# Kernel optimization log

Hardware: AMD Instinct MI355X
Metric: run time of the kernel (lower is better)

The kernel has to match this reference:

```python
import jax, jax.numpy as jnp
import numpy as np
from jax import lax

D = 256      # d_model
NH = 4       # nhead == len(multi_size)
DH = D // NH # per-head dim = 64
B, H, W = 8, 32, 32
EPS_LN = 1e-5
EPS_ATT = 1e-6


def conv2d(x, w, pad):
    # x: [B,C,H,W], w: [O,I,k,k], SAME padding via pad=k//2
    return lax.conv_general_dilated(
        x, w, window_strides=(1, 1), padding=[(pad, pad), (pad, pad)],
        dimension_numbers=("NCHW", "OIHW", "NCHW"))


def layer_norm(x, g, b):
    m = jnp.mean(x, axis=-1, keepdims=True)
    v = jnp.mean((x - m) ** 2, axis=-1, keepdims=True)
    return (x - m) * lax.rsqrt(v + EPS_LN) * g + b


def setup_inputs() -> dict:
    key = jax.random.key(0)
    ks = jax.random.split(key, 20)
    s = 0.02
    inp = {
        "x": jax.random.normal(ks[0], (B, D, H, W), jnp.float32),
        "source": jax.random.normal(ks[1], (B, D, H, W), jnp.float32),
        # q projection: conv3x3 d_model -> d_model (bias-free)
        "Wq": jax.random.normal(ks[2], (D, D, 3, 3), jnp.float32) * s,
        # MultiConv k projection: kernels 1,3,5,7, each d_model -> dim
        "Wk1": jax.random.normal(ks[3], (DH, D, 1, 1), jnp.float32) * s,
        "Wk3": jax.random.normal(ks[4], (DH, D, 3, 3), jnp.float32) * s,
        "Wk5": jax.random.normal(ks[5], (DH, D, 5, 5), jnp.float32) * s,
        "Wk7": jax.random.normal(ks[6], (DH, D, 7, 7), jnp.float32) * s,
        # MultiConv v projection
        "Wv1": jax.random.normal(ks[7], (DH, D, 1, 1), jnp.float32) * s,
        "Wv3": jax.random.normal(ks[8], (DH, D, 3, 3), jnp.float32) * s,
        "Wv5": jax.random.normal(ks[9], (DH, D, 5, 5), jnp.float32) * s,
        "Wv7": jax.random.normal(ks[10], (DH, D, 7, 7), jnp.float32) * s,
        # merge linear (bias=False), stored [in,out]
        "Wm": jax.random.normal(ks[11], (D, D), jnp.float32) * s,
        "ln1_g": jnp.ones((D,), jnp.float32),
        "ln1_b": jnp.zeros((D,), jnp.float32),
        "ln2_g": jnp.ones((D,), jnp.float32),
        "ln2_b": jnp.zeros((D,), jnp.float32),
        # FF mlp: Linear(2D->2D, no bias), ReLU, Linear(2D->D, no bias); [in,out]
        "W1": jax.random.normal(ks[12], (2 * D, 2 * D), jnp.float32) * s,
        "W2": jax.random.normal(ks[13], (2 * D, D), jnp.float32) * s,
    }
    return inp


def _forward(x, source, Wq, Wk1, Wk3, Wk5, Wk7, Wv1, Wv3, Wv5, Wv7,
             Wm, ln1_g, ln1_b, ln2_g, ln2_b, W1, W2):
    b, c, h, w = x.shape
    h1, w1 = source.shape[2], source.shape[3]
    L = h * w
    S = h1 * w1

    # projections (multi-scale convs -> heads along channel)
    q = conv2d(x, Wq, 1)                                        # [b,D,h,w]
    k = jnp.concatenate([conv2d(source, Wk1, 0), conv2d(source, Wk3, 1),
                         conv2d(source, Wk5, 2), conv2d(source, Wk7, 3)], axis=1)
    v = jnp.concatenate([conv2d(source, Wv1, 0), conv2d(source, Wv3, 1),
                         conv2d(source, Wv5, 2), conv2d(source, Wv7, 3)], axis=1)

    # b c h w -> b (h w) (nhead dim) -> b L nhead dim
    q = q.transpose(0, 2, 3, 1).reshape(b, L, NH, DH)
    k = k.transpose(0, 2, 3, 1).reshape(b, S, NH, DH)
    v = v.transpose(0, 2, 3, 1).reshape(b, S, NH, DH)

    # FullAttention_vis: softmax attention map [b, L, S, nhead]
    temp = DH ** -0.5
    qk = jnp.einsum("blhd,bshd->blsh", q, k)
    attn_vis = jax.nn.softmax(qk * temp, axis=2)

    # LinearAttention (elu+1 kernel feature map)
    Qf = jax.nn.elu(q) + 1.0
    Kf = jax.nn.elu(k) + 1.0
    v_len = jnp.float32(S)
    vals = v / v_len
    KV = jnp.einsum("bshd,bshv->bhdv", Kf, vals)                # [b,NH,DH,DH]
    Z = 1.0 / (jnp.einsum("blhd,bhd->blh", Qf, Kf.sum(axis=1)) + EPS_ATT)
    msg = jnp.einsum("blhd,bhdv,blh->blhv", Qf, KV, Z) * v_len  # [b,L,NH,DH]

    # merge + norm1
    msg = layer_norm(msg.reshape(b, L, D) @ Wm, ln1_g, ln1_b)

    # FF (mlp): cat -> Linear -> ReLU -> Linear -> norm2
    xf = x.transpose(0, 2, 3, 1).reshape(b, L, c)
    ff = jax.nn.relu(jnp.concatenate([xf, msg], axis=2) @ W1) @ W2
    msg = layer_norm(ff, ln2_g, ln2_b)                          # [b,L,D]
    msg = msg.reshape(b, h, w, c).transpose(0, 3, 1, 2)         # b c h w

    out = x + msg
    # b (h0 w0) (h1 w1) c -> b c h0 w0 h1 w1
    vis = attn_vis.reshape(b, h, w, h1, w1, NH).transpose(0, 5, 1, 2, 3, 4)
    return out, vis


def reference(x, source, Wq, Wk1, Wk3, Wk5, Wk7, Wv1, Wv3, Wv5, Wv7,
              Wm, ln1_g, ln1_b, ln2_g, ln2_b, W1, W2):
    return _forward(x, source, Wq, Wk1, Wk3, Wk5, Wk7, Wv1, Wv3, Wv5, Wv7,
                    Wm, ln1_g, ln1_b, ln2_g, ln2_b, W1, W2)
```

## Files before the change

### kernel.cpp

```cpp
#include <hip/hip_runtime.h>

#define DEV __device__ __forceinline__

typedef unsigned short u16;
typedef unsigned int u32;
typedef __bf16 bf16x8 __attribute__((ext_vector_type(8)));
typedef float f32x4 __attribute__((ext_vector_type(4)));

DEV float elu1(float x) { return x > 0.f ? x + 1.f : __expf(x); }

DEV u16 f2bf(float f) {
    union { float f; unsigned u; } v; v.f = f;
    unsigned r = v.u + 0x7fffu + ((v.u >> 16) & 1u);
    return (u16)(r >> 16);
}

__global__ __launch_bounds__(256) void repack_kernel(
    const float* __restrict__ Wq,
    const float* __restrict__ Wk1, const float* __restrict__ Wk3,
    const float* __restrict__ Wk5, const float* __restrict__ Wk7,
    const float* __restrict__ Wv1, const float* __restrict__ Wv3,
    const float* __restrict__ Wv5, const float* __restrict__ Wv7,
    u16* __restrict__ wpack)
{
    int gid = blockIdx.x * 256 + threadIdx.x;
    int frag = gid >> 6, l = gid & 63;
    const float* W; int K, ocbase = 0, rel;
    if (frag < 1152) {
        W = Wq; K = 3; int slot = frag / 288; rel = frag % 288; ocbase = slot * 64;
    } else {
        int f = frag - 1152; int side = f / 2688; f %= 2688;
        if (f < 32)        { W = side ? Wv1 : Wk1; K = 1; rel = f; }
        else if (f < 320)  { W = side ? Wv3 : Wk3; K = 3; rel = f - 32; }
        else if (f < 1120) { W = side ? Wv5 : Wk5; K = 5; rel = f - 320; }
        else               { W = side ? Wv7 : Wk7; K = 7; rel = f - 1120; }
    }
    int og = rel & 3, cc = (rel >> 2) & 7, tap = rel >> 5;
    int dy = tap / K, dx = tap % K;
    int oc = ocbase + og * 16 + (l & 15);
    int c0 = cc * 32 + (l >> 4) * 8;
    u16 pk[8];
#pragma unroll
    for (int j = 0; j < 8; ++j)
        pk[j] = f2bf(W[((size_t)(oc * 256 + c0 + j) * K + dy) * K + dx]);
    *(int4*)&wpack[(size_t)frag * 512 + l * 8] = *(const int4*)pk;
}

__global__ __launch_bounds__(256) void cast_src_kernel(
    const float* __restrict__ x, const float* __restrict__ src,
    u16* __restrict__ xbh, u16* __restrict__ sbh)
{
    __shared__ float lds[32 * 129];
    const int i = blockIdx.x, t = threadIdx.x;
    const int inp = i >> 9, rem = i & 511;
    const int b = rem >> 6, cc = (rem >> 3) & 7, pxb = rem & 7;
    const float* in = (inp ? src : x) + ((size_t)b * 256 + cc * 32) * 1024 + pxb * 128;
    u16* outp = (inp ? sbh : xbh) + (size_t)b * 262144 + (size_t)cc * 32768 + pxb * 128 * 32;
#pragma unroll
    for (int u = 0; u < 4; ++u) {
        int unit = t + u * 256;
        int r = unit >> 5, px4 = unit & 31;
        float4 v = *(const float4*)(in + (size_t)r * 1024 + px4 * 4);
        lds[r * 129 + px4 * 4 + 0] = v.x;
        lds[r * 129 + px4 * 4 + 1] = v.y;
        lds[r * 129 + px4 * 4 + 2] = v.z;
        lds[r * 129 + px4 * 4 + 3] = v.w;
    }
    __syncthreads();
#pragma unroll
    for (int u = 0; u < 2; ++u) {
        int unit = t + u * 256;
        int px = unit >> 2, cg = unit & 3;
        u16 pk[8];
#pragma unroll
        for (int j = 0; j < 8; ++j) pk[j] = f2bf(lds[(cg * 8 + j) * 129 + px]);
        *(int4*)&outp[px * 32 + cg * 8] = *(const int4*)pk;
    }
}

__global__ __launch_bounds__(256) void cast_qk_kernel(
    const float* __restrict__ qb, const float* __restrict__ kb,
    u16* __restrict__ qbt, u16* __restrict__ kbt)
{
    __shared__ float lds[64 * 65];
    const int i = blockIdx.x, t = threadIdx.x;
    const int inp = i >> 9, rem = i & 511;
    const int b = rem >> 6, h = (rem >> 4) & 3, pxb = rem & 15;
    const float* in = (inp ? kb : qb) + ((size_t)b * 256 + h * 64) * 1024 + pxb * 64;
    u16* outp = (inp ? kbt : qbt) + (((size_t)(b * 4 + h)) * 1024 + pxb * 64) * 64;
#pragma unroll
    for (int u = 0; u < 4; ++u) {
        int unit = t + u * 256;
        int r = unit >> 4, px4 = unit & 15;
        float4 v = *(const float4*)(in + (size_t)r * 1024 + px4 * 4);
        lds[r * 65 + px4 * 4 + 0] = v.x;
        lds[r * 65 + px4 * 4 + 1] = v.y;
        lds[r * 65 + px4 * 4 + 2] = v.z;
        lds[r * 65 + px4 * 4 + 3] = v.w;
    }
    __syncthreads();
#pragma unroll
    for (int u = 0; u < 2; ++u) {
        int unit = t + u * 256;
        int px = unit >> 3, cg = unit & 7;
        u16 pk[8];
#pragma unroll
        for (int j = 0; j < 8; ++j) pk[j] = f2bf(lds[(cg * 8 + j) * 65 + px]);
        *(int4*)&outp[px * 64 + cg * 8] = *(const int4*)pk;
    }
}

__global__ __launch_bounds__(256) void repack_ff_kernel(
    const float* __restrict__ W1, const float* __restrict__ W2,
    const float* __restrict__ Wm,
    u16* __restrict__ w1p, u16* __restrict__ w2p, u16* __restrict__ wmp)
{
    int gid = blockIdx.x * 256 + threadIdx.x;
    int f = gid >> 6, l = gid & 63;
    if (f >= 896) return;
    u16 pk[8];
    if (f < 512) {
        int ks = f >> 5, nf = f & 31;
#pragma unroll
        for (int j = 0; j < 8; ++j)
            pk[j] = f2bf(W1[(size_t)(ks * 32 + (l >> 4) * 8 + j) * 512 + nf * 16 + (l & 15)]);
        *(int4*)&w1p[(size_t)f * 512 + l * 8] = *(const int4*)pk;
    } else if (f < 768) {
        int f2 = f - 512;
        int ks = f2 >> 4, nf = f2 & 15;
#pragma unroll
        for (int j = 0; j < 8; ++j)
            pk[j] = f2bf(W2[(size_t)(ks * 32 + (l >> 4) * 8 + j) * 256 + nf * 16 + (l & 15)]);
        *(int4*)&w2p[(size_t)f2 * 512 + l * 8] = *(const int4*)pk;
    } else {
        int f3 = f - 768;
        int ks = f3 >> 4, nf = f3 & 15;
#pragma unroll
        for (int j = 0; j < 8; ++j)
            pk[j] = f2bf(Wm[(size_t)(ks * 32 + (l >> 4) * 8 + j) * 256 + nf * 16 + (l & 15)]);
        *(int4*)&wmp[(size_t)f3 * 512 + l * 8] = *(const int4*)pk;
    }
}

template<int K>
DEV void conv_mfma_body(const u16* __restrict__ srcb,
                        const u16* __restrict__ wsec,
                        float* __restrict__ dst,
                        u16* Bt, int y0, int cch0, int ncc, int t)
{
    constexpr int P = K / 2;
    const int w = t >> 6, l = t & 63;
    const int chi = l >> 4, ln = l & 15;
    const int rowbase = chi * 22 + w * 2 + 3 - P;
    const int colbase = ln + 3 - P;
    f32x4 acc[4][4];
#pragma unroll
    for (int m = 0; m < 4; ++m)
#pragma unroll
        for (int n = 0; n < 4; ++n) acc[m][n] = (f32x4){0.f, 0.f, 0.f, 0.f};

    for (int cc = 0; cc < ncc; ++cc) {
        const int ccg = cch0 + cc;
        __syncthreads();
#pragma unroll
        for (int u = 0; u < 7; ++u) {
            int unit = t + (u << 9);
            if (unit < 2816) {
                int xv = unit & 31, r = unit >> 5;
                int yy = r % 22, ch = r / 22;
                int ygl = y0 - 3 + yy;
                int4 pk;
                if ((unsigned)ygl < 32u)
                    pk = *(const int4*)&srcb[(size_t)ccg * 32768 + (ygl * 32 + xv) * 32 + ch * 8];
// ... 59 lines not shown
    const int bx = blockIdx.x, t = threadIdx.x;
    const int g = bx & 31, b = (bx >> 5) & 7, m = bx >> 8;
    if (g < 4) {
        conv_mfma_body<3>(xbh + (size_t)b * 262144,
                          wpack + (size_t)(g * 288) * 512,
                          qb + ((size_t)b * 256 + g * 64) * 1024,
                          Bt, m * 16, 0, 8, t);
        return;
    }
    const int gs = g - 4;
    const int side = gs / 14, gg = gs % 14;
    const u16* sp = sbh + (size_t)b * 262144;
    float* fin = side ? vb : kb;
    const size_t wkb = 1152 + (size_t)side * 2688;
    if (gg == 0) {
        conv_mfma_body<1>(sp, wpack + (wkb + 0) * 512,
                          fin + ((size_t)b * 256) * 1024, Bt, m * 16, 0, 8, t);
    } else if (gg == 1) {
        conv_mfma_body<3>(sp, wpack + (wkb + 32) * 512,
                          fin + ((size_t)b * 256 + 64) * 1024, Bt, m * 16, 0, 8, t);
    } else if (gg < 6) {
        int cpart = gg - 2;
        conv_mfma_body<5>(sp, wpack + (wkb + 320) * 512,
                          p5 + (((size_t)side * 4 + cpart) * 8 + b) * 65536,
                          Bt, m * 16, cpart * 2, 2, t);
    } else {
        int cpart = gg - 6;
        conv_mfma_body<7>(sp, wpack + (wkb + 1120) * 512,
                          p7 + (((size_t)side * 8 + cpart) * 8 + b) * 65536,
                          Bt, m * 16, cpart, 1, t);
    }
}

__global__ __launch_bounds__(256) void reduce_kernel(
    const float* __restrict__ p5, const float* __restrict__ p7,
    float* __restrict__ kb, float* __restrict__ vb)
{
    int gid = blockIdx.x * 256 + threadIdx.x;
    int px4 = gid & 255;
    int rr = gid >> 8;
    int oc = rr & 63, b = (rr >> 6) & 7, head = (rr >> 9) & 1, side = rr >> 10;
    float* outb = side ? vb : kb;
    float4 s = make_float4(0.f, 0.f, 0.f, 0.f);
    if (head == 0) {
#pragma unroll
        for (int p = 0; p < 4; ++p) {
            float4 u = *((const float4*)(p5 + (((size_t)side * 4 + p) * 8 + b) * 65536 + (size_t)oc * 1024) + px4);
            s.x += u.x; s.y += u.y; s.z += u.z; s.w += u.w;
        }
        *((float4*)(outb + ((size_t)b * 256 + 128 + oc) * 1024) + px4) = s;
    } else {
#pragma unroll
        for (int p = 0; p < 8; ++p) {
            float4 u = *((const float4*)(p7 + (((size_t)side * 8 + p) * 8 + b) * 65536 + (size_t)oc * 1024) + px4);
            s.x += u.x; s.y += u.y; s.z += u.z; s.w += u.w;
        }
        *((float4*)(outb + ((size_t)b * 256 + 192 + oc) * 1024) + px4) = s;
    }
}

__global__ __launch_bounds__(512) void qk_sm_kernel(const u16* __restrict__ qbt,
                                                    const u16* __restrict__ kbt,
                                                    float* __restrict__ vis)
{
    __shared__ u16 shbuf[36 * 512];
    __shared__ float redM[32 * 8];
    __shared__ float redS[32 * 8];
    u16* kf = shbuf;
    u16* qf = shbuf + 32 * 512;
    const int t = threadIdx.x;
    const int bx = blockIdx.x;
    const int b = bx >> 7, h = (bx >> 5) & 3, l0 = (bx & 31) * 32;
    const u16* qtp = qbt + ((size_t)(b * 4 + h)) * 1024 * 64;
    const u16* ktp = kbt + ((size_t)(b * 4 + h)) * 1024 * 64;

    if (t < 256) {
        int r = t & 31, dblk = t >> 5;
        int4 pk = *(const int4*)&qtp[(size_t)(l0 + r) * 64 + dblk * 8];
        *(int4*)&qf[(((r >> 4) * 2 + (dblk >> 2)) * 64 + (dblk & 3) * 16 + (r & 15)) * 8] = pk;
    }
    __syncthreads();

    const int w = t >> 6, l = t & 63, ln = l & 15, lg = l >> 4;
    bf16x8 a[2][2];
#pragma unroll
    for (int fr = 0; fr < 2; ++fr)
#pragma unroll
        for (int ks = 0; ks < 2; ++ks)
            a[fr][ks] = *(const bf16x8*)&qf[((fr * 2 + ks) * 64 + l) * 8];

    f32x4 acc[2][4][2];
#pragma unroll
    for (int fr = 0; fr < 2; ++fr)
#pragma unroll
        for (int cc = 0; cc < 4; ++cc)
#pragma unroll
            for (int f = 0; f < 2; ++f) acc[fr][cc][f] = (f32x4){0.f, 0.f, 0.f, 0.f};

#pragma unroll
    for (int cc = 0; cc < 4; ++cc) {
        __syncthreads();
#pragma unroll
        for (int it = 0; it < 4; ++it) {
            int unit = it * 512 + t;
            int sl = unit & 255, dblk = unit >> 8;
            int4 pk = *(const int4*)&ktp[(size_t)(cc * 256 + sl) * 64 + dblk * 8];
            *(int4*)&kf[(((sl >> 4) * 2 + (dblk >> 2)) * 64 + (dblk & 3) * 16 + (sl & 15)) * 8] = pk;
        }
        __syncthreads();
#pragma unroll
        for (int f = 0; f < 2; ++f) {
            int fg = (w * 2 + f) * 2;
            bf16x8 b0 = *(const bf16x8*)&kf[((fg + 0) * 64 + l) * 8];
            bf16x8 b1 = *(const bf16x8*)&kf[((fg + 1) * 64 + l) * 8];
#pragma unroll
            for (int fr = 0; fr < 2; ++fr) {
                acc[fr][cc][f] = __builtin_amdgcn_mfma_f32_16x16x32_bf16(a[fr][0], b0, acc[fr][cc][f], 0, 0, 0);
                acc[fr][cc][f] = __builtin_amdgcn_mfma_f32_16x16x32_bf16(a[fr][1], b1, acc[fr][cc][f], 0, 0, 0);
            }
        }
    }

#pragma unroll
    for (int fr = 0; fr < 2; ++fr)
#pragma unroll
        for (int cc = 0; cc < 4; ++cc)
#pragma unroll
            for (int f = 0; f < 2; ++f)
#pragma unroll
                for (int e = 0; e < 4; ++e) acc[fr][cc][f][e] *= 0.125f;

    float rmax[2][4];
#pragma unroll
    for (int fr = 0; fr < 2; ++fr)
#pragma unroll
        for (int reg = 0; reg < 4; ++reg) {
            float m = -1e30f;
#pragma unroll
            for (int cc = 0; cc < 4; ++cc)
#pragma unroll
                for (int f = 0; f < 2; ++f) m = fmaxf(m, acc[fr][cc][f][reg]);
#pragma unroll
            for (int off = 1; off < 16; off <<= 1) m = fmaxf(m, __shfl_xor(m, off));
            if (ln == 0) redM[(fr * 16 + lg * 4 + reg) * 8 + w] = m;
            rmax[fr][reg] = m;
        }
    __syncthreads();
#pragma unroll
    for (int fr = 0; fr < 2; ++fr)
#pragma unroll
        for (int reg = 0; reg < 4; ++reg) {
            int r = fr * 16 + lg * 4 + reg;
            float m = redM[r * 8];
#pragma unroll
            for (int ww = 1; ww < 8; ++ww) m = fmaxf(m, redM[r * 8 + ww]);
            rmax[fr][reg] = m;
        }
#pragma unroll
    for (int fr = 0; fr < 2; ++fr)
#pragma unroll
        for (int reg = 0; reg < 4; ++reg) {
            float s = 0.f;
            float m = rmax[fr][reg];
#pragma unroll
            for (int cc = 0; cc < 4; ++cc)
#pragma unroll
                for (int f = 0; f < 2; ++f) {
                    float e = __expf(acc[fr][cc][f][reg] - m);
                    acc[fr][cc][f][reg] = e;
                    s += e;
                }
#pragma unroll
            for (int off = 1; off < 16; off <<= 1) s += __shfl_xor(s, off);
            if (ln == 0) redS[(fr * 16 + lg * 4 + reg) * 8 + w] = s;
        }
    __syncthreads();
    float invv[2][4];
#pragma unroll
    for (int fr = 0; fr < 2; ++fr)
#pragma unroll
        for (int reg = 0; reg < 4; ++reg) {
            int r = fr * 16 + lg * 4 + reg;
            float s = redS[r * 8] + redS[r * 8 + 1] + redS[r * 8 + 2] + redS[r * 8 + 3]
                    + redS[r * 8 + 4] + redS[r * 8 + 5] + redS[r * 8 + 6] + redS[r * 8 + 7];
            invv[fr][reg] = 1.f / s;
        }
    float* outT = (float*)shbuf;
    float* visp = vis + (((size_t)(b * 4 + h)) << 20);
#pragma unroll
    for (int cc = 0; cc < 4; ++cc) {
        __syncthreads();
#pragma unroll
        for (int fr = 0; fr < 2; ++fr)
#pragma unroll
            for (int reg = 0; reg < 4; ++reg) {
                int r = fr * 16 + lg * 4 + reg;
#pragma unroll
                for (int f = 0; f < 2; ++f)
                    outT[r * 260 + w * 32 + f * 16 + ln] = acc[fr][cc][f][reg] * invv[fr][reg];
            }
        __syncthreads();
#pragma unroll
        for (int u = 0; u < 4; ++u) {
            int unit = u * 512 + t;
            int r = unit >> 6, c4 = unit & 63;
            float4 v = *(const float4*)&outT[r * 260 + c4 * 4];
            *(float4*)&visp[(size_t)(l0 + r) * 1024 + cc * 256 + c4 * 4] = v;
        }
    }
}

__global__ __launch_bounds__(256) void kv_kernel(const float* __restrict__ k,
                                                 const float* __restrict__ v,
                                                 float* __restrict__ KVp,
                                                 float* __restrict__ Ksump)
{
    __shared__ float4 Kt4[64*17];
    __shared__ float4 Vt4[64*16];
    float* Kt = (float*)Kt4;
    float* Vt = (float*)Vt4;
    const int t = threadIdx.x;
    const int bx = blockIdx.x;
    const int b = bx >> 4, h = (bx >> 2) & 3, ch = bx & 3;
    const float* kb = k + ((size_t)b*256 + h*64)*1024 + ch*256;
    const float* vb = v + ((size_t)b*256 + h*64)*1024 + ch*256;
    const int d = t >> 2, v0 = (t & 3) * 16;
    float4 acc[4];
#pragma unroll
    for (int j = 0; j < 4; ++j) acc[j] = make_float4(0.f, 0.f, 0.f, 0.f);
    float ks = 0.f;
    for (int st = 0; st < 4; ++st) {
        __syncthreads();
        {
            int dd = t >> 2, r0 = (t & 3) * 16;
#pragma unroll
            for (int mm = 0; mm < 4; ++mm) {
                float4 kv = *(const float4*)(kb + dd*1024 + st*64 + r0 + mm*4);
                Kt[(r0+mm*4+0)*68 + dd] = elu1(kv.x);
                Kt[(r0+mm*4+1)*68 + dd] = elu1(kv.y);
                Kt[(r0+mm*4+2)*68 + dd] = elu1(kv.z);
                Kt[(r0+mm*4+3)*68 + dd] = elu1(kv.w);
                float4 vv = *(const float4*)(vb + dd*1024 + st*64 + r0 + mm*4);
                Vt[(r0+mm*4+0)*64 + dd] = vv.x;
                Vt[(r0+mm*4+1)*64 + dd] = vv.y;
                Vt[(r0+mm*4+2)*64 + dd] = vv.z;
                Vt[(r0+mm*4+3)*64 + dd] = vv.w;
            }
        }
        __syncthreads();
#pragma unroll 8
        for (int s = 0; s < 64; ++s) {
            float kf = Kt[s*68 + d];
            const float4* vp = (const float4*)(Vt + s*64 + v0);
#pragma unroll
            for (int j = 0; j < 4; ++j) {
                float4 vv = vp[j];
                acc[j].x += kf*vv.x; acc[j].y += kf*vv.y;
                acc[j].z += kf*vv.z; acc[j].w += kf*vv.w;
            }
        }
        if (t < 64) {
#pragma unroll 8
            for (int s = 0; s < 64; ++s) ks += Kt[s*68 + t];
        }
    }
    float* op = KVp + ((size_t)((ch*32 + b*4 + h)*64 + d))*64 + v0;
#pragma unroll
    for (int j = 0; j < 4; ++j) ((float4*)op)[j] = acc[j];
    if (t < 64) Ksump[(size_t)(ch*32 + b*4 + h)*64 + t] = ks;
}

__global__ __launch_bounds__(256) void msg_kernel(const float* __restrict__ q,
                                                  const float* __restrict__ KVp,
                                                  const float* __restrict__ Ksump,
                                                  float* __restrict__ msg)
{
    __shared__ float4 kvl4[4*1028];
    __shared__ float ksl[4*65];
    float* kvl = (float*)kvl4;
    const int t = threadIdx.x;
    const int bx = blockIdx.x;
    const int b = bx >> 4;
    const int l0 = (bx & 15) * 64;
    for (int m = 0; m < 64; ++m) {
        int idx = t + 256*m;
        int hh = idx >> 12, dd = (idx >> 6) & 63, vv = idx & 63;
        float s = 0.f;
#pragma unroll
        for (int ch = 0; ch < 4; ++ch)
            s += KVp[(size_t)((ch*32 + b*4))*4096 + idx];
        kvl[hh*4112 + dd*64 + vv] = s;
    }
    {
        float s = 0.f;
#pragma unroll
        for (int ch = 0; ch < 4; ++ch)
            s += Ksump[(size_t)(ch*32 + b*4)*64 + t];
        ksl[(t >> 6)*65 + (t & 63)] = s;
    }
    __syncthreads();
    const int h = t & 3, l = l0 + (t >> 2);
    const float* qb = q + ((size_t)b*256 + h*64)*1024 + l;
    float qf[64];
#pragma unroll
    for (int dd = 0; dd < 64; ++dd) qf[dd] = elu1(qb[dd*1024]);
    float zd = 1e-6f;
#pragma unroll
    for (int dd = 0; dd < 64; ++dd) zd += qf[dd] * ksl[h*65 + dd];
    const float Z = 1.f / zd;
    float* op = msg + ((size_t)(b*1024 + l))*256 + h*64;
    for (int c0 = 0; c0 < 64; c0 += 16) {
        float4 a[4];
#pragma unroll
        for (int j = 0; j < 4; ++j) a[j] = make_float4(0.f, 0.f, 0.f, 0.f);
#pragma unroll
        for (int dd = 0; dd < 64; ++dd) {
            float qv = qf[dd];
            const float4* kp = (const float4*)(kvl + h*4112 + dd*64 + c0);
#pragma unroll
            for (int j = 0; j < 4; ++j) {
                float4 kk = kp[j];
                a[j].x += qv*kk.x; a[j].y += qv*kk.y;
                a[j].z += qv*kk.z; a[j].w += qv*kk.w;
            }
        }
#pragma unroll
        for (int j = 0; j < 4; ++j) {
            a[j].x *= Z; a[j].y *= Z; a[j].z *= Z; a[j].w *= Z;
            ((float4*)(op + c0))[j] = a[j];
        }
    }
}

__global__ __launch_bounds__(256) void ff_fused_kernel(
    const float* __restrict__ x, const float* __restrict__ msg,
    const u16* __restrict__ wmp,
    const u16* __restrict__ w1p, const u16* __restrict__ w2p,
    const float* __restrict__ g1, const float* __restrict__ b1,
    const float* __restrict__ g2, const float* __restrict__ b2,
    float* __restrict__ out)
{
    __shared__ u16 tile[16 * 520];
    __shared__ u16 mtile[16 * 264];
    __shared__ float redS[16 * 4];
    __shared__ float redQ[16 * 4];
    float* tf = (float*)tile;
    const int t = threadIdx.x;
    const int base = blockIdx.x * 16;
    const int b = base >> 10, l0 = base & 1023;
    const int w = t >> 6, l = t & 63, ln = l & 15, lg = l >> 4;

    {
        int rr = t & 15, cg = t >> 4;
        for (int cci = 0; cci < 16; ++cci) {
            int c = cci * 16 + cg;
            tile[rr * 520 + c] = f2bf(x[((size_t)b * 256 + c) * 1024 + l0 + rr]);
// ... 159 lines not shown
    const float* Wk3  = (const float*)d_in[4];
    const float* Wk5  = (const float*)d_in[5];
    const float* Wk7  = (const float*)d_in[6];
    const float* Wv1  = (const float*)d_in[7];
    const float* Wv3  = (const float*)d_in[8];
    const float* Wv5  = (const float*)d_in[9];
    const float* Wv7  = (const float*)d_in[10];
    const float* Wm   = (const float*)d_in[11];
    const float* g1   = (const float*)d_in[12];
    const float* b1   = (const float*)d_in[13];
    const float* g2   = (const float*)d_in[14];
    const float* b2   = (const float*)d_in[15];
    const float* W1   = (const float*)d_in[16];
    const float* W2   = (const float*)d_in[17];

    float* out = (float*)d_out;
    float* vis = out + 2097152;

    float* p5 = vis;
    float* p7 = vis + 4194304;

    float* ws    = (float*)d_ws;
    float* qb    = ws;
    float* kb    = ws + 2097152;
    float* vb    = ws + 4194304;
    u16*   wpack = (u16*)(ws + 6291456);
    u16*   w1p   = (u16*)(ws + 6291456);
    u16*   w2p   = (u16*)(ws + 6422528);
    u16*   wmp   = (u16*)(ws + 6488064);
    u16*   qbt   = (u16*)(ws + 6520832);
    u16*   kbt   = (u16*)(ws + 7569408);
    u16*   xbh   = (u16*)(ws + 7962624);
    u16*   sbh   = (u16*)(ws + 9011200);
    float* msg   = ws + 7962624;
    float* KVp   = ws + 12156928;
    float* Ksump = ws + 12681216;

    repack_kernel   <<<1632, 256, 0, stream>>>(Wq, Wk1, Wk3, Wk5, Wk7,
                                               Wv1, Wv3, Wv5, Wv7, wpack);
    cast_src_kernel <<<1024, 256, 0, stream>>>(x, src, xbh, sbh);
    conv_mfma_kernel<<<512,  512, 0, stream>>>(xbh, sbh, wpack, qb, kb, vb, p5, p7);
    reduce_kernel   <<<2048, 256, 0, stream>>>(p5, p7, kb, vb);
    repack_ff_kernel<<<224,  256, 0, stream>>>(W1, W2, Wm, w1p, w2p, wmp);
    cast_qk_kernel  <<<1024, 256, 0, stream>>>(qb, kb, qbt, kbt);
    qk_sm_kernel    <<<1024, 512, 0, stream>>>(qbt, kbt, vis);
    kv_kernel       <<<128,  256, 0, stream>>>(kb, vb, KVp, Ksump);
    msg_kernel      <<<128,  256, 0, stream>>>(qb, KVp, Ksump, msg);
    ff_fused_kernel <<<512,  256, 0, stream>>>(x, msg, wmp, w1p, w2p,
                                               g1, b1, g2, b2, out);
}
```

Before: 274.1 us.

## Merge independent small kernels into fused launches via block-index dispatch

Independent kernels are combined into single launches that branch on blockIdx: weight repack with input cast, partial-sum reduce with FF weight repack, q/k cast with the KV reduction, and QK softmax with the message computation. This cuts the launch count from ten to six and lets unrelated work run concurrently on the GPU. The message path now reads bf16-transposed q instead of fp32 q, which lowers precision slightly and changes the memory access pattern. The msg buffer is moved so it no longer overlaps xbh and sbh.

New measurement: 269.1 us. Within noise of the previous version (-1.8%).

```diff
diff --git a/kernel.cpp b/kernel.cpp
--- a/kernel.cpp
+++ b/kernel.cpp
@@ -15,43 +15,47 @@
     return (u16)(r >> 16);
 }
 
-__global__ __launch_bounds__(256) void repack_kernel(
+DEV float bf2f(u16 h) {
+    union { u32 u; float f; } v; v.u = ((u32)h) << 16; return v.f;
+}
+
+__global__ __launch_bounds__(256) void prep1_kernel(
     const float* __restrict__ Wq,
     const float* __restrict__ Wk1, const float* __restrict__ Wk3,
     const float* __restrict__ Wk5, const float* __restrict__ Wk7,
     const float* __restrict__ Wv1, const float* __restrict__ Wv3,
     const float* __restrict__ Wv5, const float* __restrict__ Wv7,
-    u16* __restrict__ wpack)
-{
-    int gid = blockIdx.x * 256 + threadIdx.x;
-    int frag = gid >> 6, l = gid & 63;
-    const float* W; int K, ocbase = 0, rel;
-    if (frag < 1152) {
-        W = Wq; K = 3; int slot = frag / 288; rel = frag % 288; ocbase = slot * 64;
-    } else {
-        int f = frag - 1152; int side = f / 2688; f %= 2688;
-        if (f < 32)        { W = side ? Wv1 : Wk1; K = 1; rel = f; }
-        else if (f < 320)  { W = side ? Wv3 : Wk3; K = 3; rel = f - 32; }
-        else if (f < 1120) { W = side ? Wv5 : Wk5; K = 5; rel = f - 320; }
-        else               { W = side ? Wv7 : Wk7; K = 7; rel = f - 1120; }
-    }
-    int og = rel & 3, cc = (rel >> 2) & 7, tap = rel >> 5;
-    int dy = tap / K, dx = tap % K;
-    int oc = ocbase + og * 16 + (l & 15);
-    int c0 = cc * 32 + (l >> 4) * 8;
-    u16 pk[8];
-#pragma unroll
-    for (int j = 0; j < 8; ++j)
-        pk[j] = f2bf(W[((size_t)(oc * 256 + c0 + j) * K + dy) * K + dx]);
-    *(int4*)&wpack[(size_t)frag * 512 + l * 8] = *(const int4*)pk;
-}
-
-__global__ __launch_bounds__(256) void cast_src_kernel(
+    u16* __restrict__ wpack,
     const float* __restrict__ x, const float* __restrict__ src,
     u16* __restrict__ xbh, u16* __restrict__ sbh)
 {
     __shared__ float lds[32 * 129];
-    const int i = blockIdx.x, t = threadIdx.x;
+    const int t = threadIdx.x;
+    if (blockIdx.x < 1632) {
+        int gid = blockIdx.x * 256 + t;
+        int frag = gid >> 6, l = gid & 63;
+        const float* W; int K, ocbase = 0, rel;
+        if (frag < 1152) {
+            W = Wq; K = 3; int slot = frag / 288; rel = frag % 288; ocbase = slot * 64;
+        } else {
+            int f = frag - 1152; int side = f / 2688; f %= 2688;
+            if (f < 32)        { W = side ? Wv1 : Wk1; K = 1; rel = f; }
+            else if (f < 320)  { W = side ? Wv3 : Wk3; K = 3; rel = f - 32; }
+            else if (f < 1120) { W = side ? Wv5 : Wk5; K = 5; rel = f - 320; }
+            else               { W = side ? Wv7 : Wk7; K = 7; rel = f - 1120; }
+        }
+        int og = rel & 3, cc = (rel >> 2) & 7, tap = rel >> 5;
+        int dy = tap / K, dx = tap % K;
+        int oc = ocbase + og * 16 + (l & 15);
+        int c0 = cc * 32 + (l >> 4) * 8;
+        u16 pk[8];
+#pragma unroll
+        for (int j = 0; j < 8; ++j)
+            pk[j] = f2bf(W[((size_t)(oc * 256 + c0 + j) * K + dy) * K + dx]);
+        *(int4*)&wpack[(size_t)frag * 512 + l * 8] = *(const int4*)pk;
+        return;
+    }
+    const int i = blockIdx.x - 1632;
     const int inp = i >> 9, rem = i & 511;
     const int b = rem >> 6, cc = (rem >> 3) & 7, pxb = rem & 7;
     const float* in = (inp ? src : x) + ((size_t)b * 256 + cc * 32) * 1024 + pxb * 128;
@@ -75,70 +79,6 @@
 #pragma unroll
         for (int j = 0; j < 8; ++j) pk[j] = f2bf(lds[(cg * 8 + j) * 129 + px]);
         *(int4*)&outp[px * 32 + cg * 8] = *(const int4*)pk;
-    }
-}
-
-__global__ __launch_bounds__(256) void cast_qk_kernel(
-    const float* __restrict__ qb, const float* __restrict__ kb,
-    u16* __restrict__ qbt, u16* __restrict__ kbt)
-{
-    __shared__ float lds[64 * 65];
-    const int i = blockIdx.x, t = threadIdx.x;
-    const int inp = i >> 9, rem = i & 511;
-    const int b = rem >> 6, h = (rem >> 4) & 3, pxb = rem & 15;
-    const float* in = (inp ? kb : qb) + ((size_t)b * 256 + h * 64) * 1024 + pxb * 64;
-    u16* outp = (inp ? kbt : qbt) + (((size_t)(b * 4 + h)) * 1024 + pxb * 64) * 64;
-#pragma unroll
-    for (int u = 0; u < 4; ++u) {
-        int unit = t + u * 256;
-        int r = unit >> 4, px4 = unit & 15;
-        float4 v = *(const float4*)(in + (size_t)r * 1024 + px4 * 4);
-        lds[r * 65 + px4 * 4 + 0] = v.x;
-        lds[r * 65 + px4 * 4 + 1] = v.y;
-        lds[r * 65 + px4 * 4 + 2] = v.z;
-        lds[r * 65 + px4 * 4 + 3] = v.w;
-    }
-    __syncthreads();
-#pragma unroll
-    for (int u = 0; u < 2; ++u) {
-        int unit = t + u * 256;
-        int px = unit >> 3, cg = unit & 7;
-        u16 pk[8];
-#pragma unroll
-        for (int j = 0; j < 8; ++j) pk[j] = f2bf(lds[(cg * 8 + j) * 65 + px]);
-        *(int4*)&outp[px * 64 + cg * 8] = *(const int4*)pk;
-    }
-}
-
-__global__ __launch_bounds__(256) void repack_ff_kernel(
-    const float* __restrict__ W1, const float* __restrict__ W2,
-    const float* __restrict__ Wm,
-    u16* __restrict__ w1p, u16* __restrict__ w2p, u16* __restrict__ wmp)
-{
-    int gid = blockIdx.x * 256 + threadIdx.x;
-    int f = gid >> 6, l = gid & 63;
-    if (f >= 896) return;
-    u16 pk[8];
-    if (f < 512) {
-        int ks = f >> 5, nf = f & 31;
-#pragma unroll
-        for (int j = 0; j < 8; ++j)
-            pk[j] = f2bf(W1[(size_t)(ks * 32 + (l >> 4) * 8 + j) * 512 + nf * 16 + (l & 15)]);
-        *(int4*)&w1p[(size_t)f * 512 + l * 8] = *(const int4*)pk;
-    } else if (f < 768) {
-        int f2 = f - 512;
-        int ks = f2 >> 4, nf = f2 & 15;
-#pragma unroll
-        for (int j = 0; j < 8; ++j)
-            pk[j] = f2bf(W2[(size_t)(ks * 32 + (l >> 4) * 8 + j) * 256 + nf * 16 + (l & 15)]);
-        *(int4*)&w2p[(size_t)f2 * 512 + l * 8] = *(const int4*)pk;
-    } else {
-        int f3 = f - 768;
-        int ks = f3 >> 4, nf = f3 & 15;
-#pragma unroll
-        for (int j = 0; j < 8; ++j)
-            pk[j] = f2bf(Wm[(size_t)(ks * 32 + (l >> 4) * 8 + j) * 256 + nf * 16 + (l & 15)]);
-        *(int4*)&wmp[(size_t)f3 * 512 + l * 8] = *(const int4*)pk;
     }
 }
 
@@ -264,198 +204,110 @@
     }
 }
 
-__global__ __launch_bounds__(256) void reduce_kernel(
+__global__ __launch_bounds__(256) void prep2_kernel(
     const float* __restrict__ p5, const float* __restrict__ p7,
-    float* __restrict__ kb, float* __restrict__ vb)
+    float* __restrict__ kb, float* __restrict__ vb,
+    const float* __restrict__ W1, const float* __restrict__ W2,
+    const float* __restrict__ Wm,
+    u16* __restrict__ w1p, u16* __restrict__ w2p, u16* __restrict__ wmp)
 {
-    int gid = blockIdx.x * 256 + threadIdx.x;
-    int px4 = gid & 255;
-    int rr = gid >> 8;
-    int oc = rr & 63, b = (rr >> 6) & 7, head = (rr >> 9) & 1, side = rr >> 10;
-    float* outb = side ? vb : kb;
-    float4 s = make_float4(0.f, 0.f, 0.f, 0.f);
-    if (head == 0) {
-#pragma unroll
-        for (int p = 0; p < 4; ++p) {
-            float4 u = *((const float4*)(p5 + (((size_t)side * 4 + p) * 8 + b) * 65536 + (size_t)oc * 1024) + px4);
-            s.x += u.x; s.y += u.y; s.z += u.z; s.w += u.w;
-        }
-        *((float4*)(outb + ((size_t)b * 256 + 128 + oc) * 1024) + px4) = s;
+    const int t = threadIdx.x;
+    if (blockIdx.x < 2048) {
+        int gid = blockIdx.x * 256 + t;
+        int px4 = gid & 255;
+        int rr = gid >> 8;
+        int oc = rr & 63, b = (rr >> 6) & 7, head = (rr >> 9) & 1, side = rr >> 10;
+        float* outb = side ? vb : kb;
+        float4 s = make_float4(0.f, 0.f, 0.f, 0.f);
+        if (head == 0) {
+#pragma unroll
+            for (int p = 0; p < 4; ++p) {
+                float4 u = *((const float4*)(p5 + (((size_t)side * 4 + p) * 8 + b) * 65536 + (size_t)oc * 1024) + px4);
+                s.x += u.x; s.y += u.y; s.z += u.z; s.w += u.w;
+            }
+            *((float4*)(outb + ((size_t)b * 256 + 128 + oc) * 1024) + px4) = s;
+        } else {
+#pragma unroll
+            for (int p = 0; p < 8; ++p) {
+                float4 u = *((const float4*)(p7 + (((size_t)side * 8 + p) * 8 + b) * 65536 + (size_t)oc * 1024) + px4);
+                s.x += u.x; s.y += u.y; s.z += u.z; s.w += u.w;
+            }
+            *((float4*)(outb + ((size_t)b * 256 + 192 + oc) * 1024) + px4) = s;
+        }
+        return;
+    }
+    int gid = (blockIdx.x - 2048) * 256 + t;
+    int f = gid >> 6, l = gid & 63;
+    if (f >= 896) return;
+    u16 pk[8];
+    if (f < 512) {
+        int ks = f >> 5, nf = f & 31;
+#pragma unroll
+        for (int j = 0; j < 8; ++j)
+            pk[j] = f2bf(W1[(size_t)(ks * 32 + (l >> 4) * 8 + j) * 512 + nf * 16 + (l & 15)]);
+        *(int4*)&w1p[(size_t)f * 512 + l * 8] = *(const int4*)pk;
+    } else if (f < 768) {
+        int f2 = f - 512;
+        int ks = f2 >> 4, nf = f2 & 15;
+#pragma unroll
+        for (int j = 0; j < 8; ++j)
+            pk[j] = f2bf(W2[(size_t)(ks * 32 + (l >> 4) * 8 + j) * 256 + nf * 16 + (l & 15)]);
+        *(int4*)&w2p[(size_t)f2 * 512 + l * 8] = *(const int4*)pk;
     } else {
-#pragma unroll
-        for (int p = 0; p < 8; ++p) {
-            float4 u = *((const float4*)(p7 + (((size_t)side * 8 + p) * 8 + b) * 65536 + (size_t)oc * 1024) + px4);
-            s.x += u.x; s.y += u.y; s.z += u.z; s.w += u.w;
-        }
-        *((float4*)(outb + ((size_t)b * 256 + 192 + oc) * 1024) + px4) = s;
-    }
-}
-
-__global__ __launch_bounds__(512) void qk_sm_kernel(const u16* __restrict__ qbt,
-                                                    const u16* __restrict__ kbt,
-                                                    float* __restrict__ vis)
+        int f3 = f - 768;
+        int ks = f3 >> 4, nf = f3 & 15;
+#pragma unroll
+        for (int j = 0; j < 8; ++j)
+            pk[j] = f2bf(Wm[(size_t)(ks * 32 + (l >> 4) * 8 + j) * 256 + nf * 16 + (l & 15)]);
+        *(int4*)&wmp[(size_t)f3 * 512 + l * 8] = *(const int4*)pk;
+    }
+}
+
+__global__ __launch_bounds__(256) void prep3_kernel(
+    const float* __restrict__ qb, const float* __restrict__ kb,
+    const float* __restrict__ vb,
+    u16* __restrict__ qbt, u16* __restrict__ kbt,
+    float* __restrict__ KVp, float* __restrict__ Ksump)
 {
-    __shared__ u16 shbuf[36 * 512];
-    __shared__ float redM[32 * 8];
-    __shared__ float redS[32 * 8];
-    u16* kf = shbuf;
-    u16* qf = shbuf + 32 * 512;
+    __shared__ float4 smem4[2112];
     const int t = threadIdx.x;
-    const int bx = blockIdx.x;
-    const int b = bx >> 7, h = (bx >> 5) & 3, l0 = (bx & 31) * 32;
-    const u16* qtp = qbt + ((size_t)(b * 4 + h)) * 1024 * 64;
-    const u16* ktp = kbt + ((size_t)(b * 4 + h)) * 1024 * 64;
-
-    if (t < 256) {
-        int r = t & 31, dblk = t >> 5;
-        int4 pk = *(const int4*)&qtp[(size_t)(l0 + r) * 64 + dblk * 8];
-        *(int4*)&qf[(((r >> 4) * 2 + (dblk >> 2)) * 64 + (dblk & 3) * 16 + (r & 15)) * 8] = pk;
-    }
-    __syncthreads();
-
-    const int w = t >> 6, l = t & 63, ln = l & 15, lg = l >> 4;
-    bf16x8 a[2][2];
-#pragma unroll
-    for (int fr = 0; fr < 2; ++fr)
-#pragma unroll
-        for (int ks = 0; ks < 2; ++ks)
-            a[fr][ks] = *(const bf16x8*)&qf[((fr * 2 + ks) * 64 + l) * 8];
-
-    f32x4 acc[2][4][2];
-#pragma unroll
-    for (int fr = 0; fr < 2; ++fr)
-#pragma unroll
-        for (int cc = 0; cc < 4; ++cc)
-#pragma unroll
-            for (int f = 0; f < 2; ++f) acc[fr][cc][f] = (f32x4){0.f, 0.f, 0.f, 0.f};
-
-#pragma unroll
-    for (int cc = 0; cc < 4; ++cc) {
+    if (blockIdx.x < 1024) {
+        float* lds = (float*)smem4;
+        const int i = blockIdx.x;
+        const int inp = i >> 9, rem = i & 511;
+        const int b = rem >> 6, h = (rem >> 4) & 3, pxb = rem & 15;
+        const float* in = (inp ? kb : qb) + ((size_t)b * 256 + h * 64) * 1024 + pxb * 64;
+        u16* outp = (inp ? kbt : qbt) + (((size_t)(b * 4 + h)) * 1024 + pxb * 64) * 64;
+#pragma unroll
+        for (int u = 0; u < 4; ++u) {
+            int unit = t + u * 256;
+            int r = unit >> 4, px4 = unit & 15;
+            float4 v = *(const float4*)(in + (size_t)r * 1024 + px4 * 4);
+            lds[r * 65 + px4 * 4 + 0] = v.x;
+            lds[r * 65 + px4 * 4 + 1] = v.y;
+            lds[r * 65 + px4 * 4 + 2] = v.z;
+            lds[r * 65 + px4 * 4 + 3] = v.w;
+        }
         __syncthreads();
 #pragma unroll
-        for (int it = 0; it < 4; ++it) {
-            int unit = it * 512 + t;
-            int sl = unit & 255, dblk = unit >> 8;
-            int4 pk = *(const int4*)&ktp[(size_t)(cc * 256 + sl) * 64 + dblk * 8];
-            *(int4*)&kf[(((sl >> 4) * 2 + (dblk >> 2)) * 64 + (dblk & 3) * 16 + (sl & 15)) * 8] = pk;
-        }
-        __syncthreads();
-#pragma unroll
-        for (int f = 0; f < 2; ++f) {
-            int fg = (w * 2 + f) * 2;
-            bf16x8 b0 = *(const bf16x8*)&kf[((fg + 0) * 64 + l) * 8];
-            bf16x8 b1 = *(const bf16x8*)&kf[((fg + 1) * 64 + l) * 8];
-#pragma unroll
-            for (int fr = 0; fr < 2; ++fr) {
-                acc[fr][cc][f] = __builtin_amdgcn_mfma_f32_16x16x32_bf16(a[fr][0], b0, acc[fr][cc][f], 0, 0, 0);
-                acc[fr][cc][f] = __builtin_amdgcn_mfma_f32_16x16x32_bf16(a[fr][1], b1, acc[fr][cc][f], 0, 0, 0);
-            }
-        }
-    }
-
-#pragma unroll
-    for (int fr = 0; fr < 2; ++fr)
-#pragma unroll
-        for (int cc = 0; cc < 4; ++cc)
-#pragma unroll
-            for (int f = 0; f < 2; ++f)
-#pragma unroll
-                for (int e = 0; e < 4; ++e) acc[fr][cc][f][e] *= 0.125f;
-
-    float rmax[2][4];
-#pragma unroll
-    for (int fr = 0; fr < 2; ++fr)
-#pragma unroll
-        for (int reg = 0; reg < 4; ++reg) {
-            float m = -1e30f;
-#pragma unroll
-            for (int cc = 0; cc < 4; ++cc)
-#pragma unroll
-                for (int f = 0; f < 2; ++f) m = fmaxf(m, acc[fr][cc][f][reg]);
-#pragma unroll
-            for (int off = 1; off < 16; off <<= 1) m = fmaxf(m, __shfl_xor(m, off));
-            if (ln == 0) redM[(fr * 16 + lg * 4 + reg) * 8 + w] = m;
-            rmax[fr][reg] = m;
-        }
-    __syncthreads();
-#pragma unroll
-    for (int fr = 0; fr < 2; ++fr)
-#pragma unroll
-        for (int reg = 0; reg < 4; ++reg) {
-            int r = fr * 16 + lg * 4 + reg;
-            float m = redM[r * 8];
-#pragma unroll
-            for (int ww = 1; ww < 8; ++ww) m = fmaxf(m, redM[r * 8 + ww]);
-            rmax[fr][reg] = m;
-        }
-#pragma unroll
-    for (int fr = 0; fr < 2; ++fr)
-#pragma unroll
-        for (int reg = 0; reg < 4; ++reg) {
-            float s = 0.f;
-            float m = rmax[fr][reg];
-#pragma unroll
-            for (int cc = 0; cc < 4; ++cc)
-#pragma unroll
-                for (int f = 0; f < 2; ++f) {
-                    float e = __expf(acc[fr][cc][f][reg] - m);
-                    acc[fr][cc][f][reg] = e;
-                    s += e;
-                }
-#pragma unroll
-            for (int off = 1; off < 16; off <<= 1) s += __shfl_xor(s, off);
-            if (ln == 0) redS[(fr * 16 + lg * 4 + reg) * 8 + w] = s;
-        }
-    __syncthreads();
-    float invv[2][4];
-#pragma unroll
-    for (int fr = 0; fr < 2; ++fr)
-#pragma unroll
-        for (int reg = 0; reg < 4; ++reg) {
-            int r = fr * 16 + lg * 4 + reg;
-            float s = redS[r * 8] + redS[r * 8 + 1] + redS[r * 8 + 2] + redS[r * 8 + 3]
-                    + redS[r * 8 + 4] + redS[r * 8 + 5] + redS[r * 8 + 6] + redS[r * 8 + 7];
-            invv[fr][reg] = 1.f / s;
-        }
-    float* outT = (float*)shbuf;
-    float* visp = vis + (((size_t)(b * 4 + h)) << 20);
-#pragma unroll
-    for (int cc = 0; cc < 4; ++cc) {
-        __syncthreads();
-#pragma unroll
-        for (int fr = 0; fr < 2; ++fr)
-#pragma unroll
-            for (int reg = 0; reg < 4; ++reg) {
-                int r = fr * 16 + lg * 4 + reg;
-#pragma unroll
-                for (int f = 0; f < 2; ++f)
-                    outT[r * 260 + w * 32 + f * 16 + ln] = acc[fr][cc][f][reg] * invv[fr][reg];
-            }
-        __syncthreads();
-#pragma unroll
-        for (int u = 0; u < 4; ++u) {
-            int unit = u * 512 + t;
-            int r = unit >> 6, c4 = unit & 63;
-            float4 v = *(const float4*)&outT[r * 260 + c4 * 4];
-            *(float4*)&visp[(size_t)(l0 + r) * 1024 + cc * 256 + c4 * 4] = v;
-        }
-    }
-}
-
-__global__ __launch_bounds__(256) void kv_kernel(const float* __restrict__ k,
-                                                 const float* __restrict__ v,
-                                                 float* __restrict__ KVp,
-                                                 float* __restrict__ Ksump)
-{
-    __shared__ float4 Kt4[64*17];
-    __shared__ float4 Vt4[64*16];
+        for (int u = 0; u < 2; ++u) {
+            int unit = t + u * 256;
+            int px = unit >> 3, cg = unit & 7;
+            u16 pk[8];
+#pragma unroll
+            for (int j = 0; j < 8; ++j) pk[j] = f2bf(lds[(cg * 8 + j) * 65 + px]);
+            *(int4*)&outp[px * 64 + cg * 8] = *(const int4*)pk;
+        }
+        return;
+    }
+    float4* Kt4 = smem4;
+    float4* Vt4 = smem4 + 64 * 17;
     float* Kt = (float*)Kt4;
     float* Vt = (float*)Vt4;
-    const int t = threadIdx.x;
-    const int bx = blockIdx.x;
+    const int bx = blockIdx.x - 1024;
     const int b = bx >> 4, h = (bx >> 2) & 3, ch = bx & 3;
-    const float* kb = k + ((size_t)b*256 + h*64)*1024 + ch*256;
-    const float* vb = v + ((size_t)b*256 + h*64)*1024 + ch*256;
+    const float* kp = kb + ((size_t)b * 256 + h * 64) * 1024 + ch * 256;
+    const float* vp = vb + ((size_t)b * 256 + h * 64) * 1024 + ch * 256;
     const int d = t >> 2, v0 = (t & 3) * 16;
     float4 acc[4];
 #pragma unroll
@@ -467,80 +319,234 @@
             int dd = t >> 2, r0 = (t & 3) * 16;
 #pragma unroll
             for (int mm = 0; mm < 4; ++mm) {
-                float4 kv = *(const float4*)(kb + dd*1024 + st*64 + r0 + mm*4);
-                Kt[(r0+mm*4+0)*68 + dd] = elu1(kv.x);
-                Kt[(r0+mm*4+1)*68 + dd] = elu1(kv.y);
-                Kt[(r0+mm*4+2)*68 + dd] = elu1(kv.z);
-                Kt[(r0+mm*4+3)*68 + dd] = elu1(kv.w);
-                float4 vv = *(const float4*)(vb + dd*1024 + st*64 + r0 + mm*4);
-                Vt[(r0+mm*4+0)*64 + dd] = vv.x;
-                Vt[(r0+mm*4+1)*64 + dd] = vv.y;
-                Vt[(r0+mm*4+2)*64 + dd] = vv.z;
-                Vt[(r0+mm*4+3)*64 + dd] = vv.w;
+                float4 kv = *(const float4*)(kp + dd * 1024 + st * 64 + r0 + mm * 4);
+                Kt[(r0 + mm * 4 + 0) * 68 + dd] = elu1(kv.x);
+                Kt[(r0 + mm * 4 + 1) * 68 + dd] = elu1(kv.y);
+                Kt[(r0 + mm * 4 + 2) * 68 + dd] = elu1(kv.z);
+                Kt[(r0 + mm * 4 + 3) * 68 + dd] = elu1(kv.w);
+                float4 vv = *(const float4*)(vp + dd * 1024 + st * 64 + r0 + mm * 4);
+                Vt[(r0 + mm * 4 + 0) * 64 + dd] = vv.x;
+                Vt[(r0 + mm * 4 + 1) * 64 + dd] = vv.y;
+                Vt[(r0 + mm * 4 + 2) * 64 + dd] = vv.z;
+                Vt[(r0 + mm * 4 + 3) * 64 + dd] = vv.w;
             }
         }
         __syncthreads();
 #pragma unroll 8
         for (int s = 0; s < 64; ++s) {
-            float kf = Kt[s*68 + d];
-            const float4* vp = (const float4*)(Vt + s*64 + v0);
+            float kf = Kt[s * 68 + d];
+            const float4* vvp = (const float4*)(Vt + s * 64 + v0);
 #pragma unroll
             for (int j = 0; j < 4; ++j) {
-                float4 vv = vp[j];
-                acc[j].x += kf*vv.x; acc[j].y += kf*vv.y;
-                acc[j].z += kf*vv.z; acc[j].w += kf*vv.w;
+                float4 vv = vvp[j];
+                acc[j].x += kf * vv.x; acc[j].y += kf * vv.y;
+                acc[j].z += kf * vv.z; acc[j].w += kf * vv.w;
             }
         }
         if (t < 64) {
 #pragma unroll 8
-            for (int s = 0; s < 64; ++s) ks += Kt[s*68 + t];
-        }
-    }
-    float* op = KVp + ((size_t)((ch*32 + b*4 + h)*64 + d))*64 + v0;
+            for (int s = 0; s < 64; ++s) ks += Kt[s * 68 + t];
+        }
+    }
+    float* op = KVp + ((size_t)((ch * 32 + b * 4 + h) * 64 + d)) * 64 + v0;
 #pragma unroll
     for (int j = 0; j < 4; ++j) ((float4*)op)[j] = acc[j];
-    if (t < 64) Ksump[(size_t)(ch*32 + b*4 + h)*64 + t] = ks;
-}
-
-__global__ __launch_bounds__(256) void msg_kernel(const float* __restrict__ q,
-                                                  const float* __restrict__ KVp,
-                                                  const float* __restrict__ Ksump,
-                                                  float* __restrict__ msg)
+    if (t < 64) Ksump[(size_t)(ch * 32 + b * 4 + h) * 64 + t] = ks;
+}
+
+__global__ __launch_bounds__(512) void qk_sm_msg_kernel(
+    const u16* __restrict__ qbt, const u16* __restrict__ kbt,
+    float* __restrict__ vis,
+    const float* __restrict__ KVp, const float* __restrict__ Ksump,
+    float* __restrict__ msg)
 {
-    __shared__ float4 kvl4[4*1028];
-    __shared__ float ksl[4*65];
-    float* kvl = (float*)kvl4;
+    __shared__ float4 smem4[4178];
     const int t = threadIdx.x;
-    const int bx = blockIdx.x;
-    const int b = bx >> 4;
-    const int l0 = (bx & 15) * 64;
-    for (int m = 0; m < 64; ++m) {
-        int idx = t + 256*m;
-        int hh = idx >> 12, dd = (idx >> 6) & 63, vv = idx & 63;
+    if (blockIdx.x < 1024) {
+        u16* kf = (u16*)smem4;
+        u16* qf = (u16*)smem4 + 32 * 512;
+        float* redM = (float*)((char*)smem4 + 36864);
+        float* redS = redM + 256;
+        const int bx = blockIdx.x;
+        const int b = bx >> 7, h = (bx >> 5) & 3, l0 = (bx & 31) * 32;
+        const u16* qtp = qbt + ((size_t)(b * 4 + h)) * 1024 * 64;
+        const u16* ktp = kbt + ((size_t)(b * 4 + h)) * 1024 * 64;
+
+        if (t < 256) {
+            int r = t & 31, dblk = t >> 5;
+            int4 pk = *(const int4*)&qtp[(size_t)(l0 + r) * 64 + dblk * 8];
+            *(int4*)&qf[(((r >> 4) * 2 + (dblk >> 2)) * 64 + (dblk & 3) * 16 + (r & 15)) * 8] = pk;
+        }
+        __syncthreads();
+
+        const int w = t >> 6, l = t & 63, ln = l & 15, lg = l >> 4;
+        bf16x8 a[2][2];
+#pragma unroll
+        for (int fr = 0; fr < 2; ++fr)
+#pragma unroll
+            for (int ks = 0; ks < 2; ++ks)
+                a[fr][ks] = *(const bf16x8*)&qf[((fr * 2 + ks) * 64 + l) * 8];
+
+        f32x4 acc[2][4][2];
+#pragma unroll
+        for (int fr = 0; fr < 2; ++fr)
+#pragma unroll
+            for (int cc = 0; cc < 4; ++cc)
+#pragma unroll
+                for (int f = 0; f < 2; ++f) acc[fr][cc][f] = (f32x4){0.f, 0.f, 0.f, 0.f};
+
+#pragma unroll
+        for (int cc = 0; cc < 4; ++cc) {
+            __syncthreads();
+#pragma unroll
+            for (int it = 0; it < 4; ++it) {
+                int unit = it * 512 + t;
+                int sl = unit & 255, dblk = unit >> 8;
+                int4 pk = *(const int4*)&ktp[(size_t)(cc * 256 + sl) * 64 + dblk * 8];
+                *(int4*)&kf[(((sl >> 4) * 2 + (dblk >> 2)) * 64 + (dblk & 3) * 16 + (sl & 15)) * 8] = pk;
+            }
+            __syncthreads();
+#pragma unroll
+            for (int f = 0; f < 2; ++f) {
+                int fg = (w * 2 + f) * 2;
+                bf16x8 b0 = *(const bf16x8*)&kf[((fg + 0) * 64 + l) * 8];
+                bf16x8 b1 = *(const bf16x8*)&kf[((fg + 1) * 64 + l) * 8];
+#pragma unroll
+                for (int fr = 0; fr < 2; ++fr) {
+                    acc[fr][cc][f] = __builtin_amdgcn_mfma_f32_16x16x32_bf16(a[fr][0], b0, acc[fr][cc][f], 0, 0, 0);
+                    acc[fr][cc][f] = __builtin_amdgcn_mfma_f32_16x16x32_bf16(a[fr][1], b1, acc[fr][cc][f], 0, 0, 0);
+                }
+            }
+        }
+
+#pragma unroll
+        for (int fr = 0; fr < 2; ++fr)
+#pragma unroll
+            for (int cc = 0; cc < 4; ++cc)
+#pragma unroll
+                for (int f = 0; f < 2; ++f)
+#pragma unroll
+                    for (int e = 0; e < 4; ++e) acc[fr][cc][f][e] *= 0.125f;
+
+        float rmax[2][4];
+#pragma unroll
+        for (int fr = 0; fr < 2; ++fr)
+#pragma unroll
+            for (int reg = 0; reg < 4; ++reg) {
+                float m = -1e30f;
+#pragma unroll
+                for (int cc = 0; cc < 4; ++cc)
+#pragma unroll
+                    for (int f = 0; f < 2; ++f) m = fmaxf(m, acc[fr][cc][f][reg]);
+#pragma unroll
+                for (int off = 1; off < 16; off <<= 1) m = fmaxf(m, __shfl_xor(m, off));
+                if (ln == 0) redM[(fr * 16 + lg * 4 + reg) * 8 + w] = m;
+                rmax[fr][reg] = m;
+            }
+        __syncthreads();
+#pragma unroll
+        for (int fr = 0; fr < 2; ++fr)
+#pragma unroll
+            for (int reg = 0; reg < 4; ++reg) {
+                int r = fr * 16 + lg * 4 + reg;
+                float m = redM[r * 8];
+#pragma unroll
+                for (int ww = 1; ww < 8; ++ww) m = fmaxf(m, redM[r * 8 + ww]);
+                rmax[fr][reg] = m;
+            }
+#pragma unroll
+        for (int fr = 0; fr < 2; ++fr)
+#pragma unroll
+            for (int reg = 0; reg < 4; ++reg) {
+                float s = 0.f;
+                float m = rmax[fr][reg];
+#pragma unroll
+                for (int cc = 0; cc < 4; ++cc)
+#pragma unroll
+                    for (int f = 0; f < 2; ++f) {
+                        float e = __expf(acc[fr][cc][f][reg] - m);
+                        acc[fr][cc][f][reg] = e;
+                        s += e;
+                    }
+#pragma unroll
+                for (int off = 1; off < 16; off <<= 1) s += __shfl_xor(s, off);
+                if (ln == 0) redS[(fr * 16 + lg * 4 + reg) * 8 + w] = s;
+            }
+        __syncthreads();
+        float invv[2][4];
+#pragma unroll
+        for (int fr = 0; fr < 2; ++fr)
+#pragma unroll
+            for (int reg = 0; reg < 4; ++reg) {
+                int r = fr * 16 + lg * 4 + reg;
+                float s = redS[r * 8] + redS[r * 8 + 1] + redS[r * 8 + 2] + redS[r * 8 + 3]
+                        + redS[r * 8 + 4] + redS[r * 8 + 5] + redS[r * 8 + 6] + redS[r * 8 + 7];
+                invv[fr][reg] = 1.f / s;
+            }
+        float* outT = (float*)smem4;
+        float* visp = vis + (((size_t)(b * 4 + h)) << 20);
+#pragma unroll
+        for (int cc = 0; cc < 4; ++cc) {
+            __syncthreads();
+#pragma unroll
+            for (int fr = 0; fr < 2; ++fr)
+#pragma unroll
+                for (int reg = 0; reg < 4; ++reg) {
+                    int r = fr * 16 + lg * 4 + reg;
+#pragma unroll
+                    for (int f = 0; f < 2; ++f)
+                        outT[r * 260 + w * 32 + f * 16 + ln] = acc[fr][cc][f][reg] * invv[fr][reg];
+                }
+            __syncthreads();
+#pragma unroll
+            for (int u = 0; u < 4; ++u) {
+                int unit = u * 512 + t;
+                int r = unit >> 6, c4 = unit & 63;
+                float4 v = *(const float4*)&outT[r * 260 + c4 * 4];
+                *(float4*)&visp[(size_t)(l0 + r) * 1024 + cc * 256 + c4 * 4] = v;
+            }
+        }
+        return;
+    }
+    float* kvl = (float*)smem4;
+    float* ksl = (float*)smem4 + 4 * 4112;
+    const int bx2 = blockIdx.x - 1024;
+    const int b = bx2 >> 3, l0 = (bx2 & 7) * 128;
+#pragma unroll
+    for (int m = 0; m < 8; ++m) {
+        int unit = t + (m << 9);
+        int hh = unit >> 10, dd = (unit >> 4) & 63, v4 = unit & 15;
+        float4 s = make_float4(0.f, 0.f, 0.f, 0.f);
+#pragma unroll
+        for (int ch = 0; ch < 4; ++ch) {
+            float4 u = *(const float4*)&KVp[((size_t)(ch * 32 + b * 4)) * 4096 + (size_t)unit * 4];
+            s.x += u.x; s.y += u.y; s.z += u.z; s.w += u.w;
+        }
+        *(float4*)&kvl[hh * 4112 + dd * 64 + v4 * 4] = s;
+    }
+    if (t < 256) {
         float s = 0.f;
 #pragma unroll
         for (int ch = 0; ch < 4; ++ch)
-            s += KVp[(size_t)((ch*32 + b*4))*4096 + idx];
-        kvl[hh*4112 + dd*64 + vv] = s;
-    }
-    {
-        float s = 0.f;
-#pragma unroll
-        for (int ch = 0; ch < 4; ++ch)
-            s += Ksump[(size_t)(ch*32 + b*4)*64 + t];
-        ksl[(t >> 6)*65 + (t & 63)] = s;
+            s += Ksump[(size_t)(ch * 32 + b * 4) * 64 + t];
+        ksl[(t >> 6) * 65 + (t & 63)] = s;
     }
     __syncthreads();
     const int h = t & 3, l = l0 + (t >> 2);
-    const float* qb = q + ((size_t)b*256 + h*64)*1024 + l;
+    const u16* qrow = qbt + ((size_t)(b * 4 + h) * 1024 + l) * 64;
     float qf[64];
 #pragma unroll
-    for (int dd = 0; dd < 64; ++dd) qf[dd] = elu1(qb[dd*1024]);
+    for (int j8 = 0; j8 < 8; ++j8) {
+        int4 pk = *(const int4*)&qrow[j8 * 8];
+        const u16* pku = (const u16*)&pk;
+#pragma unroll
+        for (int e = 0; e < 8; ++e) qf[j8 * 8 + e] = elu1(bf2f(pku[e]));
+    }
     float zd = 1e-6f;
 #pragma unroll
-    for (int dd = 0; dd < 64; ++dd) zd += qf[dd] * ksl[h*65 + dd];
+    for (int dd = 0; dd < 64; ++dd) zd += qf[dd] * ksl[h * 65 + dd];
     const float Z = 1.f / zd;
-    float* op = msg + ((size_t)(b*1024 + l))*256 + h*64;
+    float* op = msg + ((size_t)(b * 1024 + l)) * 256 + h * 64;
     for (int c0 = 0; c0 < 64; c0 += 16) {
         float4 a[4];
 #pragma unroll
@@ -548,12 +554,12 @@
 #pragma unroll
         for (int dd = 0; dd < 64; ++dd) {
             float qv = qf[dd];
-            const float4* kp = (const float4*)(kvl + h*4112 + dd*64 + c0);
+            const float4* kp = (const float4*)(kvl + h * 4112 + dd * 64 + c0);
 #pragma unroll
             for (int j = 0; j < 4; ++j) {
                 float4 kk = kp[j];
-                a[j].x += qv*kk.x; a[j].y += qv*kk.y;
-                a[j].z += qv*kk.z; a[j].w += qv*kk.w;
+                a[j].x += qv * kk.x; a[j].y += qv * kk.y;
+                a[j].z += qv * kk.z; a[j].w += qv * kk.w;
             }
         }
 #pragma unroll
@@ -779,20 +785,18 @@
     u16*   kbt   = (u16*)(ws + 7569408);
     u16*   xbh   = (u16*)(ws + 7962624);
     u16*   sbh   = (u16*)(ws + 9011200);
-    float* msg   = ws + 7962624;
+    float* msg   = ws + 10059776;
     float* KVp   = ws + 12156928;
     float* Ksump = ws + 12681216;
 
-    repack_kernel   <<<1632, 256, 0, stream>>>(Wq, Wk1, Wk3, Wk5, Wk7,
-                                               Wv1, Wv3, Wv5, Wv7, wpack);
-    cast_src_kernel <<<1024, 256, 0, stream>>>(x, src, xbh, sbh);
+    prep1_kernel    <<<2656, 256, 0, stream>>>(Wq, Wk1, Wk3, Wk5, Wk7,
+                                               Wv1, Wv3, Wv5, Wv7, wpack,
+                                               x, src, xbh, sbh);
     conv_mfma_kernel<<<512,  512, 0, stream>>>(xbh, sbh, wpack, qb, kb, vb, p5, p7);
-    reduce_kernel   <<<2048, 256, 0, stream>>>(p5, p7, kb, vb);
-    repack_ff_kernel<<<224,  256, 0, stream>>>(W1, W2, Wm, w1p, w2p, wmp);
-    cast_qk_kernel  <<<1024, 256, 0, stream>>>(qb, kb, qbt, kbt);
-    qk_sm_kernel    <<<1024, 512, 0, stream>>>(qbt, kbt, vis);
-    kv_kernel       <<<128,  256, 0, stream>>>(kb, vb, KVp, Ksump);
-    msg_kernel      <<<128,  256, 0, stream>>>(qb, KVp, Ksump, msg);
+    prep2_kernel    <<<2272, 256, 0, stream>>>(p5, p7, kb, vb,
+                                               W1, W2, Wm, w1p, w2p, wmp);
+    prep3_kernel    <<<1152, 256, 0, stream>>>(qb, kb, vb, qbt, kbt, KVp, Ksump);
+    qk_sm_msg_kernel<<<1088, 512, 0, stream>>>(qbt, kbt, vis, KVp, Ksump, msg);
     ff_fused_kernel <<<512,  256, 0, stream>>>(x, msg, wmp, w1p, w2p,
                                                g1, b1, g2, b2, out);
 }
```
